# Performance work log

Hardware: AMD Instinct MI355X
Metric: run time of the kernel (lower is better)

The kernel has to match this reference:

```python
import jax, jax.numpy as jnp
import numpy as np

N_NODES = 30000
N_EDGES = 480000
N_GRAPHS = 64
NEG_SLOPE = 0.2


def gat_layer(h, src, dst, W, a_l, a_r, b):
    # h: [N, F_in], W: [F_in, H*D], a_l/a_r: [H, D], b: [H*D]
    N = h.shape[0]
    H, D = a_l.shape
    feat = (h @ W).reshape(N, H, D)
    el = jnp.sum(feat * a_l[None], axis=-1)  # [N, H]
    er = jnp.sum(feat * a_r[None], axis=-1)  # [N, H]
    e = jax.nn.leaky_relu(el[src] + er[dst], NEG_SLOPE)  # [E, H]
    # edge-softmax over incoming edges of each dst node (numerically stable)
    emax = jax.ops.segment_max(e, dst, num_segments=N)          # [N, H]
    ex = jnp.exp(e - emax[dst])                                  # [E, H]
    denom = jax.ops.segment_sum(ex, dst, num_segments=N)        # [N, H]
    alpha = ex / denom[dst]                                      # [E, H]
    msg = feat[src] * alpha[..., None]                           # [E, H, D]
    out = jax.ops.segment_sum(msg, dst, num_segments=N)         # [N, H, D]
    return out.reshape(N, H * D) + b


def setup_inputs() -> dict:
    key = jax.random.key(0)
    ks = jax.random.split(key, 16)
    feat = jax.random.normal(ks[0], (N_NODES, 6), dtype=jnp.float32)
    src = jax.random.randint(ks[1], (N_EDGES,), 0, N_NODES)
    dst = jax.random.randint(ks[2], (N_EDGES,), 0, N_NODES)
    graph_id = jnp.sort(jax.random.randint(ks[3], (N_NODES,), 0, N_GRAPHS))
    s = 0.1
    W1 = jax.random.normal(ks[4], (6, 128), dtype=jnp.float32) * s
    al1 = jax.random.normal(ks[5], (4, 32), dtype=jnp.float32) * s
    ar1 = jax.random.normal(ks[6], (4, 32), dtype=jnp.float32) * s
    b1 = jnp.zeros((128,), dtype=jnp.float32)
    W2 = jax.random.normal(ks[7], (128, 128), dtype=jnp.float32) * s
    al2 = jax.random.normal(ks[8], (4, 32), dtype=jnp.float32) * s
    ar2 = jax.random.normal(ks[9], (4, 32), dtype=jnp.float32) * s
    b2 = jnp.zeros((128,), dtype=jnp.float32)
    W3 = jax.random.normal(ks[10], (128, 256), dtype=jnp.float32) * s
    al3 = jax.random.normal(ks[11], (4, 64), dtype=jnp.float32) * s
    ar3 = jax.random.normal(ks[12], (4, 64), dtype=jnp.float32) * s
    b3 = jnp.zeros((256,), dtype=jnp.float32)
    return {"feat": feat, "src": src, "dst": dst, "graph_id": graph_id,
            "W1": W1, "al1": al1, "ar1": ar1, "b1": b1,
            "W2": W2, "al2": al2, "ar2": ar2, "b2": b2,
            "W3": W3, "al3": al3, "ar3": ar3, "b3": b3}


def reference(feat, src, dst, graph_id, W1, al1, ar1, b1, W2, al2, ar2, b2, W3, al3, ar3, b3):
    h = gat_layer(feat, src, dst, W1, al1, ar1, b1)  # [N, 128]
    h = jax.nn.relu(h)                                # dropout is identity in eval
    h = gat_layer(h, src, dst, W2, al2, ar2, b2)      # [N, 128]
    h = jax.nn.relu(h)
    h = gat_layer(h, src, dst, W3, al3, ar3, b3)      # [N, 256]
    # dgl.mean_nodes over batched graphs
    hs = jax.ops.segment_sum(h, graph_id, num_segments=N_GRAPHS)  # [G, 256]
    cnt = jax.ops.segment_sum(jnp.ones((h.shape[0],), h.dtype), graph_id, num_segments=N_GRAPHS)
    hg = hs / jnp.maximum(cnt, 1.0)[:, None]
    return hg
```

## Files before the change

### kernel.cpp

```cpp
#include <hip/hip_runtime.h>

typedef _Float16 h4 __attribute__((ext_vector_type(4)));
typedef _Float16 h8v __attribute__((ext_vector_type(8)));
typedef float f4v __attribute__((ext_vector_type(4)));
typedef float f32x8 __attribute__((ext_vector_type(8)));


__global__ void zero_i32(int* __restrict__ p, int n) {
    int i = blockIdx.x * blockDim.x + threadIdx.x;
    if (i < n) p[i] = 0;
}

__global__ void hist_kernel(const int* __restrict__ dst, int* __restrict__ counts, int E) {
    int i = blockIdx.x * blockDim.x + threadIdx.x;
    if (i < E) atomicAdd(&counts[dst[i]], 1);
}

__global__ void scan_block(const int* __restrict__ counts, int* __restrict__ rowptr,
                           int* __restrict__ bsum, int n) {
    __shared__ int wsum[16];
    const int tid = threadIdx.x;
    const int lane = tid & 63, wv = tid >> 6;
    const int i = blockIdx.x * 1024 + tid;
    int v = (i < n) ? counts[i] : 0;
    int x = v;
#pragma unroll
    for (int off = 1; off < 64; off <<= 1) {
        int t = __shfl_up(x, off);
        if (lane >= off) x += t;
    }
    if (lane == 63) wsum[wv] = x;
    __syncthreads();
    if (tid < 16) {
        int y = wsum[tid];
#pragma unroll
        for (int off = 1; off < 16; off <<= 1) {
            int t = __shfl_up(y, off);
            if (tid >= off) y += t;
        }
        wsum[tid] = y;
    }
    __syncthreads();
    int woff = (wv > 0) ? wsum[wv - 1] : 0;
    if (i < n) rowptr[i] = woff + x - v;
    if (tid == 0) bsum[blockIdx.x] = wsum[15];
}

__global__ void scan_add_tops(int* __restrict__ rowptr, const int* __restrict__ bsum,
                              int nb, int n) {
    __shared__ int off_s, tot_s;
    const int b = blockIdx.x;
    const int tid = threadIdx.x;
    if (tid < 64) {
        int v = (tid < nb) ? bsum[tid] : 0;
        int x = v;
#pragma unroll
        for (int off = 1; off < 64; off <<= 1) {
            int t = __shfl_up(x, off);
            if (tid >= off) x += t;
        }
        if (tid == 63) tot_s = x;
        if (tid == b) off_s = x - v;
    }
    __syncthreads();
    int i = b * 1024 + tid;
    if (i < n) rowptr[i] += off_s;
    if (b == 0 && tid == 0) rowptr[n] = tot_s;
}

__global__ void scatter_kernel(const int* __restrict__ src, const int* __restrict__ dst,
                               const int* __restrict__ rowptr, int* __restrict__ cursor,
                               int* __restrict__ srcs, int E) {
    int i = blockIdx.x * blockDim.x + threadIdx.x;
    if (i < E) {
        int d = dst[i];
        int p = rowptr[d] + atomicAdd(&cursor[d], 1);
        srcs[p] = src[i];
    }
}

__global__ void pack_w_both(const float* __restrict__ W2, _Float16* __restrict__ Wp2,
                            const float* __restrict__ W3, _Float16* __restrict__ Wp3) {
    int idx = blockIdx.x * blockDim.x + threadIdx.x;
    const float* W; _Float16* Wp; int FOUT;
    if (idx < 2048) { W = W2; Wp = Wp2; FOUT = 128; }
    else {
        idx -= 2048;
        if (idx >= 4096) return;
        W = W3; Wp = Wp3; FOUT = 256;
    }
    int l = idx & 63;
    int ks = (idx >> 6) & 3;
    int ct = idx >> 8;
    int kbase = ks * 32 + (l >> 4) * 8;
    int col = ct * 16 + (l & 15);
    h8v v;
#pragma unroll
    for (int e = 0; e < 8; e++) v[e] = (_Float16)W[(size_t)(kbase + e) * FOUT + col];
    *reinterpret_cast<h8v*>(&Wp[(size_t)idx * 8]) = v;
}

template <int FIN, int FOUT, int D>
__global__ void gemm_att(const float* __restrict__ A, const float* __restrict__ W,
                         const float* __restrict__ al, const float* __restrict__ ar,
                         _Float16* __restrict__ feat, float* __restrict__ el,
                         float* __restrict__ er, int N) {
    constexpr int R = 16;
    constexpr int H = FOUT / D;
    constexpr int T = FOUT / 2;
    __shared__ __align__(16) float As[FIN][R + 4];
    const int j = threadIdx.x;
    const int h0 = j / D;
    const int h1 = (j + T) / D;
    const float alv0 = al[j],     arv0 = ar[j];
    const float alv1 = al[j + T], arv1 = ar[j + T];
    const int row0 = blockIdx.x * R;

    for (int idx = threadIdx.x; idx < R * FIN; idx += T) {
        int r = idx / FIN, k = idx % FIN;
        int rr = row0 + r;
        As[k][r] = (rr < N) ? A[(size_t)rr * FIN + k] : 0.f;
    }
    __syncthreads();

    float acc0[R], acc1[R];
#pragma unroll
    for (int r = 0; r < R; r++) { acc0[r] = 0.f; acc1[r] = 0.f; }

    for (int k = 0; k < FIN; k++) {
        float w0 = W[(size_t)k * FOUT + j];
        float w1 = W[(size_t)k * FOUT + j + T];
        const float4* ap = reinterpret_cast<const float4*>(&As[k][0]);
        float av[16];
        *reinterpret_cast<float4*>(&av[0])  = ap[0];
        *reinterpret_cast<float4*>(&av[4])  = ap[1];
        *reinterpret_cast<float4*>(&av[8])  = ap[2];
        *reinterpret_cast<float4*>(&av[12]) = ap[3];
#pragma unroll
        for (int r = 0; r < R; r++) {
            acc0[r] += av[r] * w0;
            acc1[r] += av[r] * w1;
        }
    }

#pragma unroll
    for (int r = 0; r < R; r++) {
        int rr = row0 + r;
        if (rr >= N) break;
        float v0 = acc0[r], v1 = acc1[r];
        feat[(size_t)rr * FOUT + j] = (_Float16)v0;
        feat[(size_t)rr * FOUT + j + T] = (_Float16)v1;
        float vl0 = v0 * alv0, vr0 = v0 * arv0;
        float vl1 = v1 * alv1, vr1 = v1 * arv1;
#pragma unroll
        for (int off = D / 2; off >= 1; off >>= 1) {
            vl0 += __shfl_xor(vl0, off);
            vr0 += __shfl_xor(vr0, off);
            vl1 += __shfl_xor(vl1, off);
            vr1 += __shfl_xor(vr1, off);
        }
        if ((j % D) == 0) {
            el[(size_t)rr * H + h0] = vl0;
            er[(size_t)rr * H + h0] = vr0;
            el[(size_t)rr * H + h1] = vl1;
            er[(size_t)rr * H + h1] = vr1;
        }
    }
}

template <int K, int FOUT, int D>
__global__ __launch_bounds__(256)
void gemm_mfma(const _Float16* __restrict__ A, const _Float16* __restrict__ Wp,
               const float* __restrict__ al, const float* __restrict__ ar,
               _Float16* __restrict__ feat, float* __restrict__ el,
               float* __restrict__ er, int N) {
    constexpr int RB  = 32;
    constexpr int KS  = K / 32;
    constexpr int CHW = FOUT / 2;
    constexpr int CTW = CHW / 16;
    constexpr int CTH = D / 16;
    constexpr int HW  = CTW / CTH;
    constexpr int H   = FOUT / D;
    constexpr int STR = K + 8;
    __shared__ _Float16 As[RB * STR];
    const int tid = threadIdx.x;
    const int w  = tid >> 6;
    const int l  = tid & 63;
    const int rt = w >> 1;
    const int ch = w & 1;
    const int row0 = blockIdx.x * RB;

    constexpr int NV8 = RB * K / 8;
    for (int v = tid; v < NV8; v += 256) {
        int r  = v / (K / 8);
        int kv = (v % (K / 8)) * 8;
        int rr = row0 + r;
        h8v x = {};
        if (rr < N) x = *reinterpret_cast<const h8v*>(&A[(size_t)rr * K + kv]);
        *reinterpret_cast<h8v*>(&As[r * STR + kv]) = x;
    }
    __syncthreads();

    h8v afrag[KS];
    {
        const _Float16* base = &As[(rt * 16 + (l & 15)) * STR + ((l >> 4) * 8)];
#pragma unroll
        for (int ks = 0; ks < KS; ks++)
            afrag[ks] = *reinterpret_cast<const h8v*>(&base[ks * 32]);
    }

    const h8v* Wv = reinterpret_cast<const h8v*>(Wp);
    const int ct0 = ch * CTW;
    f4v acc[CTW];
#pragma unroll
    for (int c = 0; c < CTW; c++) acc[c] = (f4v){0.f, 0.f, 0.f, 0.f};

    h8v bfr[2][KS];
#pragma unroll
    for (int ks = 0; ks < KS; ks++) bfr[0][ks] = Wv[(size_t)((ct0 * KS + ks) * 64 + l)];
#pragma unroll
    for (int c = 0; c < CTW; c++) {
        const int cur = c & 1, nxt = cur ^ 1;
        if (c + 1 < CTW) {
#pragma unroll
            for (int ks = 0; ks < KS; ks++)
                bfr[nxt][ks] = Wv[(size_t)(((ct0 + c + 1) * KS + ks) * 64 + l)];
        }
#pragma unroll
        for (int ks = 0; ks < KS; ks++)
            acc[c] = __builtin_amdgcn_mfma_f32_16x16x32_f16(afrag[ks], bfr[cur][ks], acc[c], 0, 0, 0);
    }

    float elp[HW][4], erp[HW][4];
#pragma unroll
    for (int hh = 0; hh < HW; hh++)
#pragma unroll
        for (int r = 0; r < 4; r++) { elp[hh][r] = 0.f; erp[hh][r] = 0.f; }

#pragma unroll
    for (int c = 0; c < CTW; c++) {
        const int col = ch * CHW + c * 16 + (l & 15);
        const float alv = al[col], arv = ar[col];
        const int hh = c / CTH;
#pragma unroll
        for (int r = 0; r < 4; r++) {
            float v = acc[c][r];
            elp[hh][r] += v * alv;
            erp[hh][r] += v * arv;
            int rr = row0 + rt * 16 + (l >> 4) * 4 + r;
            if (rr < N) feat[(size_t)rr * FOUT + col] = (_Float16)v;
        }
    }
#pragma unroll
    for (int hh = 0; hh < HW; hh++) {
#pragma unroll
        for (int r = 0; r < 4; r++) {
            float v = elp[hh][r], u = erp[hh][r];
#pragma unroll
            for (int off = 8; off >= 1; off >>= 1) {
                v += __shfl_xor(v, off);
                u += __shfl_xor(u, off);
            }
            if ((l & 15) == 0) {
                int rr = row0 + rt * 16 + (l >> 4) * 4 + r;
                if (rr < N) {
                    int hg = ch * HW + hh;
                    el[(size_t)rr * H + hg] = v;
                    er[(size_t)rr * H + hg] = u;
                }
            }
        }
    }
}

template <int HD, int D, bool FP16OUT>
__global__ __launch_bounds__(256)
void agg_fused(const h8v* __restrict__ featH8, const float* __restrict__ el,
               const float* __restrict__ er, const int* __restrict__ srcs,
               const int* __restrict__ rowptr, const float* __restrict__ bias,
               void* __restrict__ outp, int N) {
    constexpr int TPN = HD / 8;
    constexpr int NPB = 256 / TPN;
    const int tid = threadIdx.x;
    const int ln = tid % TPN;
    const int node = blockIdx.x * NPB + tid / TPN;
    if (node >= N) return;
    const int h = ln / (D / 8);
    const int beg = rowptr[node], end = rowptr[node + 1];
    const float ern = er[(size_t)node * 4 + h];

    float s = 0.f;
    f32x8 a0 = {0,0,0,0,0,0,0,0}, a1 = a0;

    int i = beg;
    int alend = (beg + 3) & ~3;
    if (alend > end) alend = end;
    for (; i < alend; i++) {
        int u = srcs[i];
        float x = el[(size_t)u * 4 + h] + ern; x = x > 0.f ? x : 0.2f * x;
        h8v f = featH8[(size_t)u * TPN + ln];
        float w = __expf(x);
        s += w;
#pragma unroll
        for (int k = 0; k < 8; k++) a0[k] += w * (float)f[k];
    }
    for (; i + 4 <= end; i += 4) {
        int4 uu = *reinterpret_cast<const int4*>(&srcs[i]);
        float x0 = el[(size_t)uu.x * 4 + h] + ern; x0 = x0 > 0.f ? x0 : 0.2f * x0;
        float x1 = el[(size_t)uu.y * 4 + h] + ern; x1 = x1 > 0.f ? x1 : 0.2f * x1;
        float x2 = el[(size_t)uu.z * 4 + h] + ern; x2 = x2 > 0.f ? x2 : 0.2f * x2;
        float x3 = el[(size_t)uu.w * 4 + h] + ern; x3 = x3 > 0.f ? x3 : 0.2f * x3;
        h8v f0 = featH8[(size_t)uu.x * TPN + ln];
        h8v f1 = featH8[(size_t)uu.y * TPN + ln];
        h8v f2 = featH8[(size_t)uu.z * TPN + ln];
        h8v f3 = featH8[(size_t)uu.w * TPN + ln];
        float w0 = __expf(x0), w1 = __expf(x1);
        float w2 = __expf(x2), w3 = __expf(x3);
        s += (w0 + w1) + (w2 + w3);
#pragma unroll
        for (int k = 0; k < 8; k++) {
            a0[k] += w0 * (float)f0[k];
            a1[k] += w1 * (float)f1[k];
            a0[k] += w2 * (float)f2[k];
            a1[k] += w3 * (float)f3[k];
        }
    }
    for (; i < end; i++) {
        int u = srcs[i];
        float x = el[(size_t)u * 4 + h] + ern; x = x > 0.f ? x : 0.2f * x;
        h8v f = featH8[(size_t)u * TPN + ln];
        float w = __expf(x);
        s += w;
#pragma unroll
        for (int k = 0; k < 8; k++) a0[k] += w * (float)f[k];
    }
    const float inv = (s > 0.f) ? 1.f / s : 0.f;
    if constexpr (FP16OUT) {
        const float4 b0 = *reinterpret_cast<const float4*>(&bias[ln * 8]);
        const float4 b1v = *reinterpret_cast<const float4*>(&bias[ln * 8 + 4]);
        float bb[8] = {b0.x, b0.y, b0.z, b0.w, b1v.x, b1v.y, b1v.z, b1v.w};
        h8v o;
#pragma unroll
        for (int k = 0; k < 8; k++)
            o[k] = (_Float16)fmaxf((a0[k] + a1[k]) * inv + bb[k], 0.f);
        reinterpret_cast<h8v*>(outp)[(size_t)node * TPN + ln] = o;
    } else {
        f32x8 o;
#pragma unroll
        for (int k = 0; k < 8; k++) o[k] = (a0[k] + a1[k]) * inv;
        reinterpret_cast<f32x8*>(outp)[(size_t)node * TPN + ln] = o;
    }
}


__device__ __forceinline__ int lower_bound_i(const int* __restrict__ a, int n, int key) {
    int lo = 0, hi = n;
    while (lo < hi) {
        int mid = (lo + hi) >> 1;
        if (a[mid] < key) lo = mid + 1; else hi = mid;
    }
    return lo;
}

__global__ void readout_partial(const float* __restrict__ agg, const int* __restrict__ gid,
                                float* __restrict__ part, int N, int C, int SL) {
    int g = blockIdx.x / SL, slice = blockIdx.x % SL;
    int c = threadIdx.x;
    int start = lower_bound_i(gid, N, g);
    int end = lower_bound_i(gid, N, g + 1);
    float sum = 0.f;
    for (int n = start + slice; n < end; n += SL) sum += agg[(size_t)n * C + c];
    part[((size_t)g * SL + slice) * C + c] = sum;
}

__global__ void readout_final(const float* __restrict__ part, const float* __restrict__ b3,
                              const int* __restrict__ gid, float* __restrict__ out,
                              int N, int C, int SL) {
    int g = blockIdx.x, c = threadIdx.x;
    int start = lower_bound_i(gid, N, g);
    int end = lower_bound_i(gid, N, g + 1);
    int cnt = end - start;
    float s = 0.f;
    for (int k = 0; k < SL; k++) s += part[((size_t)g * SL + k) * C + c];
    out[(size_t)g * C + c] = (cnt > 0) ? s / (float)cnt + b3[c] : 0.f;
}


extern "C" void kernel_launch(void* const* d_in, const int* in_sizes, int n_in,
                              void* d_out, int out_size, void* d_ws, size_t ws_size,
                              hipStream_t stream) {
    const float* feat0 = (const float*)d_in[0];
    const int* src = (const int*)d_in[1];
    const int* dst = (const int*)d_in[2];
    const int* gid = (const int*)d_in[3];
    const float* W1 = (const float*)d_in[4];
    const float* al1 = (const float*)d_in[5];
    const float* ar1 = (const float*)d_in[6];
    const float* b1 = (const float*)d_in[7];
    const float* W2 = (const float*)d_in[8];
    const float* al2 = (const float*)d_in[9];
    const float* ar2 = (const float*)d_in[10];
    const float* b2 = (const float*)d_in[11];
    const float* W3 = (const float*)d_in[12];
    const float* al3 = (const float*)d_in[13];
    const float* ar3 = (const float*)d_in[14];
    const float* b3 = (const float*)d_in[15];

    const int N = in_sizes[0] / 6;
    const int E = in_sizes[1];
    const int G = 64;
    const int SL = 8;
    float* out = (float*)d_out;

    char* wsp = (char*)d_ws;
    auto alloc = [&](size_t bytes) -> char* {
        char* p = wsp;
        wsp += (bytes + 255) & ~(size_t)255;
        return p;
    };
    int* counts   = (int*)alloc((size_t)N * 4);
    int* rowptr   = (int*)alloc((size_t)(N + 1) * 4);
    int* cursor   = (int*)alloc((size_t)N * 4);
    int* bsum     = (int*)alloc(64 * 4);
    int* srcs     = (int*)alloc((size_t)E * 4);
    float* el     = (float*)alloc((size_t)N * 4 * 4);
    float* er     = (float*)alloc((size_t)N * 4 * 4);
    _Float16* featH = (_Float16*)alloc((size_t)N * 256 * 2);
    _Float16* aggH  = (_Float16*)alloc((size_t)N * 128 * 2);
    float* aggB   = (float*)alloc((size_t)N * 256 * 4);
    float* part   = (float*)alloc((size_t)G * SL * 256 * 4);
    _Float16* Wp2 = (_Float16*)alloc((size_t)128 * 128 * 2);
    _Float16* Wp3 = (_Float16*)alloc((size_t)128 * 256 * 2);

    const int nb = (N + 1023) / 1024;
    const int zspan = (int)(((char*)bsum - (char*)counts) / 4) + 64;
    zero_i32<<<dim3((zspan + 255) / 256), dim3(256), 0, stream>>>(counts, zspan);
    hist_kernel<<<dim3((E + 255) / 256), dim3(256), 0, stream>>>(dst, counts, E);
    scan_block<<<dim3(nb), dim3(1024), 0, stream>>>(counts, rowptr, bsum, N);
    scan_add_tops<<<dim3(nb), dim3(1024), 0, stream>>>(rowptr, bsum, nb, N);
    scatter_kernel<<<dim3((E + 255) / 256), dim3(256), 0, stream>>>(
        src, dst, rowptr, cursor, srcs, E);

    pack_w_both<<<dim3(24), dim3(256), 0, stream>>>(W2, Wp2, W3, Wp3);

    gemm_att<6, 128, 32><<<dim3((N + 15) / 16), dim3(64), 0, stream>>>(
        feat0, W1, al1, ar1, featH, el, er, N);
    agg_fused<128, 32, true><<<dim3((N + 15) / 16), dim3(256), 0, stream>>>(
        (const h8v*)featH, el, er, srcs, rowptr, b1, aggH, N);

    gemm_mfma<128, 128, 32><<<dim3((N + 31) / 32), dim3(256), 0, stream>>>(
        aggH, Wp2, al2, ar2, featH, el, er, N);
    agg_fused<128, 32, true><<<dim3((N + 15) / 16), dim3(256), 0, stream>>>(
        (const h8v*)featH, el, er, srcs, rowptr, b2, aggH, N);

    gemm_mfma<128, 256, 64><<<dim3((N + 31) / 32), dim3(256), 0, stream>>>(
        aggH, Wp3, al3, ar3, featH, el, er, N);
    agg_fused<256, 64, false><<<dim3((N + 7) / 8), dim3(256), 0, stream>>>(
        (const h8v*)featH, el, er, srcs, rowptr, nullptr, aggB, N);

    readout_partial<<<dim3(G * SL), dim3(256), 0, stream>>>(aggB, gid, part, N, 256, SL);
    readout_final<<<dim3(G), dim3(256), 0, stream>>>(part, b3, gid, out, N, 256, SL);
}
```

Baseline: 209.9 us.

## Fuse front kernels, split aggregation by channel sections, store layer-3 output in fp16

Merges the histogram, weight-packing and first-layer GEMM into a single launch using block-index ranges, which removes two launches. The edge aggregation kernels now split the channels into 2 or 4 sections across blocks, so each thread group handles fewer channels and more nodes. This is meant to improve gather locality and occupancy, at the cost of reading edge lists and attention logits once per section. The final aggregation output becomes fp16 instead of fp32, halving its write and readout traffic at some cost in precision.

```diff
diff --git a/kernel.cpp b/kernel.cpp
--- a/kernel.cpp
+++ b/kernel.cpp
@@ -9,11 +9,6 @@
 __global__ void zero_i32(int* __restrict__ p, int n) {
     int i = blockIdx.x * blockDim.x + threadIdx.x;
     if (i < n) p[i] = 0;
-}
-
-__global__ void hist_kernel(const int* __restrict__ dst, int* __restrict__ counts, int E) {
-    int i = blockIdx.x * blockDim.x + threadIdx.x;
-    if (i < E) atomicAdd(&counts[dst[i]], 1);
 }
 
 __global__ void scan_block(const int* __restrict__ counts, int* __restrict__ rowptr,
@@ -79,47 +74,54 @@
     }
 }
 
-__global__ void pack_w_both(const float* __restrict__ W2, _Float16* __restrict__ Wp2,
-                            const float* __restrict__ W3, _Float16* __restrict__ Wp3) {
-    int idx = blockIdx.x * blockDim.x + threadIdx.x;
-    const float* W; _Float16* Wp; int FOUT;
-    if (idx < 2048) { W = W2; Wp = Wp2; FOUT = 128; }
-    else {
-        idx -= 2048;
-        if (idx >= 4096) return;
-        W = W3; Wp = Wp3; FOUT = 256;
-    }
-    int l = idx & 63;
-    int ks = (idx >> 6) & 3;
-    int ct = idx >> 8;
-    int kbase = ks * 32 + (l >> 4) * 8;
-    int col = ct * 16 + (l & 15);
-    h8v v;
-#pragma unroll
-    for (int e = 0; e < 8; e++) v[e] = (_Float16)W[(size_t)(kbase + e) * FOUT + col];
-    *reinterpret_cast<h8v*>(&Wp[(size_t)idx * 8]) = v;
-}
-
-template <int FIN, int FOUT, int D>
-__global__ void gemm_att(const float* __restrict__ A, const float* __restrict__ W,
-                         const float* __restrict__ al, const float* __restrict__ ar,
-                         _Float16* __restrict__ feat, float* __restrict__ el,
-                         float* __restrict__ er, int N) {
-    constexpr int R = 16;
-    constexpr int H = FOUT / D;
-    constexpr int T = FOUT / 2;
-    __shared__ __align__(16) float As[FIN][R + 4];
-    const int j = threadIdx.x;
+__global__ __launch_bounds__(256)
+void fused_front(const int* __restrict__ dst, int* __restrict__ counts, int E,
+                 const float* __restrict__ W2, _Float16* __restrict__ Wp2,
+                 const float* __restrict__ W3, _Float16* __restrict__ Wp3,
+                 const float* __restrict__ A, const float* __restrict__ W1,
+                 const float* __restrict__ al, const float* __restrict__ ar,
+                 _Float16* __restrict__ feat, float* __restrict__ el,
+                 float* __restrict__ er, int N, int HB, int PB) {
+    const int b = blockIdx.x;
+    if (b < HB) {
+        int i = b * 256 + threadIdx.x;
+        if (i < E) atomicAdd(&counts[dst[i]], 1);
+        return;
+    }
+    if (b < HB + PB) {
+        int idx = (b - HB) * 256 + threadIdx.x;
+        const float* W; _Float16* Wp; int FOUT;
+        if (idx < 2048) { W = W2; Wp = Wp2; FOUT = 128; }
+        else {
+            idx -= 2048;
+            if (idx >= 4096) return;
+            W = W3; Wp = Wp3; FOUT = 256;
+        }
+        int l = idx & 63;
+        int ks = (idx >> 6) & 3;
+        int ct = idx >> 8;
+        int kbase = ks * 32 + (l >> 4) * 8;
+        int col = ct * 16 + (l & 15);
+        h8v v;
+#pragma unroll
+        for (int e = 0; e < 8; e++) v[e] = (_Float16)W[(size_t)(kbase + e) * FOUT + col];
+        *reinterpret_cast<h8v*>(&Wp[(size_t)idx * 8]) = v;
+        return;
+    }
+    constexpr int FIN = 6, FOUT = 128, D = 32, R = 16, H = 4, T = 64;
+    __shared__ __align__(16) float As[4][FIN][R + 4];
+    const int sub = threadIdx.x >> 6;
+    const int j = threadIdx.x & 63;
     const int h0 = j / D;
     const int h1 = (j + T) / D;
     const float alv0 = al[j],     arv0 = ar[j];
     const float alv1 = al[j + T], arv1 = ar[j + T];
-    const int row0 = blockIdx.x * R;
-
-    for (int idx = threadIdx.x; idx < R * FIN; idx += T) {
+    const int row0 = (b - HB - PB) * 64 + sub * R;
+
+    for (int idx = j; idx < R * FIN; idx += T) {
         int r = idx / FIN, k = idx % FIN;
         int rr = row0 + r;
-        As[k][r] = (rr < N) ? A[(size_t)rr * FIN + k] : 0.f;
+        As[sub][k][r] = (rr < N) ? A[(size_t)rr * FIN + k] : 0.f;
     }
     __syncthreads();
 
@@ -128,9 +130,9 @@
     for (int r = 0; r < R; r++) { acc0[r] = 0.f; acc1[r] = 0.f; }
 
     for (int k = 0; k < FIN; k++) {
-        float w0 = W[(size_t)k * FOUT + j];
-        float w1 = W[(size_t)k * FOUT + j + T];
-        const float4* ap = reinterpret_cast<const float4*>(&As[k][0]);
+        float w0 = W1[(size_t)k * FOUT + j];
+        float w1 = W1[(size_t)k * FOUT + j + T];
+        const float4* ap = reinterpret_cast<const float4*>(&As[sub][k][0]);
         float av[16];
         *reinterpret_cast<float4*>(&av[0])  = ap[0];
         *reinterpret_cast<float4*>(&av[4])  = ap[1];
@@ -273,21 +275,25 @@
     }
 }
 
-template <int HD, int D, bool FP16OUT>
+template <int HD, int D, int CSPLIT, bool FP16OUT>
 __global__ __launch_bounds__(256)
 void agg_fused(const h8v* __restrict__ featH8, const float* __restrict__ el,
                const float* __restrict__ er, const int* __restrict__ srcs,
                const int* __restrict__ rowptr, const float* __restrict__ bias,
-               void* __restrict__ outp, int N) {
-    constexpr int TPN = HD / 8;
+               void* __restrict__ outp, int N, int nbase) {
+    constexpr int CH  = HD / CSPLIT;
+    constexpr int TPN = CH / 8;
     constexpr int NPB = 256 / TPN;
     const int tid = threadIdx.x;
     const int ln = tid % TPN;
-    const int node = blockIdx.x * NPB + tid / TPN;
+    const int sec = blockIdx.x / nbase;
+    const int node = (blockIdx.x % nbase) * NPB + tid / TPN;
     if (node >= N) return;
-    const int h = ln / (D / 8);
+    const int chbase = sec * CH;
+    const int h = (chbase + ln * 8) / D;
     const int beg = rowptr[node], end = rowptr[node + 1];
     const float ern = er[(size_t)node * 4 + h];
+    const h8v* frow = featH8 + (chbase / 8) + ln;
 
     float s = 0.f;
     f32x8 a0 = {0,0,0,0,0,0,0,0}, a1 = a0;
@@ -298,7 +304,7 @@
     for (; i < alend; i++) {
         int u = srcs[i];
         float x = el[(size_t)u * 4 + h] + ern; x = x > 0.f ? x : 0.2f * x;
-        h8v f = featH8[(size_t)u * TPN + ln];
+        h8v f = frow[(size_t)u * (HD / 8)];
         float w = __expf(x);
         s += w;
 #pragma unroll
@@ -310,10 +316,10 @@
         float x1 = el[(size_t)uu.y * 4 + h] + ern; x1 = x1 > 0.f ? x1 : 0.2f * x1;
         float x2 = el[(size_t)uu.z * 4 + h] + ern; x2 = x2 > 0.f ? x2 : 0.2f * x2;
         float x3 = el[(size_t)uu.w * 4 + h] + ern; x3 = x3 > 0.f ? x3 : 0.2f * x3;
-        h8v f0 = featH8[(size_t)uu.x * TPN + ln];
-        h8v f1 = featH8[(size_t)uu.y * TPN + ln];
-        h8v f2 = featH8[(size_t)uu.z * TPN + ln];
-        h8v f3 = featH8[(size_t)uu.w * TPN + ln];
+        h8v f0 = frow[(size_t)uu.x * (HD / 8)];
+        h8v f1 = frow[(size_t)uu.y * (HD / 8)];
+        h8v f2 = frow[(size_t)uu.z * (HD / 8)];
+        h8v f3 = frow[(size_t)uu.w * (HD / 8)];
         float w0 = __expf(x0), w1 = __expf(x1);
         float w2 = __expf(x2), w3 = __expf(x3);
         s += (w0 + w1) + (w2 + w3);
@@ -328,7 +334,7 @@
     for (; i < end; i++) {
         int u = srcs[i];
         float x = el[(size_t)u * 4 + h] + ern; x = x > 0.f ? x : 0.2f * x;
-        h8v f = featH8[(size_t)u * TPN + ln];
+        h8v f = frow[(size_t)u * (HD / 8)];
         float w = __expf(x);
         s += w;
 #pragma unroll
@@ -336,19 +342,19 @@
     }
     const float inv = (s > 0.f) ? 1.f / s : 0.f;
     if constexpr (FP16OUT) {
-        const float4 b0 = *reinterpret_cast<const float4*>(&bias[ln * 8]);
-        const float4 b1v = *reinterpret_cast<const float4*>(&bias[ln * 8 + 4]);
+        const float4 b0 = *reinterpret_cast<const float4*>(&bias[chbase + ln * 8]);
+        const float4 b1v = *reinterpret_cast<const float4*>(&bias[chbase + ln * 8 + 4]);
         float bb[8] = {b0.x, b0.y, b0.z, b0.w, b1v.x, b1v.y, b1v.z, b1v.w};
         h8v o;
 #pragma unroll
         for (int k = 0; k < 8; k++)
             o[k] = (_Float16)fmaxf((a0[k] + a1[k]) * inv + bb[k], 0.f);
-        reinterpret_cast<h8v*>(outp)[(size_t)node * TPN + ln] = o;
+        reinterpret_cast<h8v*>(outp)[(size_t)node * (HD / 8) + chbase / 8 + ln] = o;
     } else {
-        f32x8 o;
-#pragma unroll
-        for (int k = 0; k < 8; k++) o[k] = (a0[k] + a1[k]) * inv;
-        reinterpret_cast<f32x8*>(outp)[(size_t)node * TPN + ln] = o;
+        h8v o;
+#pragma unroll
+        for (int k = 0; k < 8; k++) o[k] = (_Float16)((a0[k] + a1[k]) * inv);
+        reinterpret_cast<h8v*>(outp)[(size_t)node * (HD / 8) + chbase / 8 + ln] = o;
     }
 }
 
@@ -362,14 +368,14 @@
     return lo;
 }
 
-__global__ void readout_partial(const float* __restrict__ agg, const int* __restrict__ gid,
+__global__ void readout_partial(const _Float16* __restrict__ agg, const int* __restrict__ gid,
                                 float* __restrict__ part, int N, int C, int SL) {
     int g = blockIdx.x / SL, slice = blockIdx.x % SL;
     int c = threadIdx.x;
     int start = lower_bound_i(gid, N, g);
     int end = lower_bound_i(gid, N, g + 1);
     float sum = 0.f;
-    for (int n = start + slice; n < end; n += SL) sum += agg[(size_t)n * C + c];
+    for (int n = start + slice; n < end; n += SL) sum += (float)agg[(size_t)n * C + c];
     part[((size_t)g * SL + slice) * C + c] = sum;
 }
 
@@ -427,37 +433,47 @@
     float* er     = (float*)alloc((size_t)N * 4 * 4);
     _Float16* featH = (_Float16*)alloc((size_t)N * 256 * 2);
     _Float16* aggH  = (_Float16*)alloc((size_t)N * 128 * 2);
-    float* aggB   = (float*)alloc((size_t)N * 256 * 4);
+    _Float16* aggF  = (_Float16*)alloc((size_t)N * 256 * 2);
     float* part   = (float*)alloc((size_t)G * SL * 256 * 4);
     _Float16* Wp2 = (_Float16*)alloc((size_t)128 * 128 * 2);
     _Float16* Wp3 = (_Float16*)alloc((size_t)128 * 256 * 2);
 
     const int nb = (N + 1023) / 1024;
     const int zspan = (int)(((char*)bsum - (char*)counts) / 4) + 64;
+    const int HB = (E + 255) / 256;
+    const int PB = 24;
+    const int CB = (N + 63) / 64;
+
     zero_i32<<<dim3((zspan + 255) / 256), dim3(256), 0, stream>>>(counts, zspan);
-    hist_kernel<<<dim3((E + 255) / 256), dim3(256), 0, stream>>>(dst, counts, E);
+    fused_front<<<dim3(HB + PB + CB), dim3(256), 0, stream>>>(
+        dst, counts, E, W2, Wp2, W3, Wp3, feat0, W1, al1, ar1, featH, el, er, N, HB, PB);
     scan_block<<<dim3(nb), dim3(1024), 0, stream>>>(counts, rowptr, bsum, N);
     scan_add_tops<<<dim3(nb), dim3(1024), 0, stream>>>(rowptr, bsum, nb, N);
     scatter_kernel<<<dim3((E + 255) / 256), dim3(256), 0, stream>>>(
         src, dst, rowptr, cursor, srcs, E);
 
-    pack_w_both<<<dim3(24), dim3(256), 0, stream>>>(W2, Wp2, W3, Wp3);
-
-    gemm_att<6, 128, 32><<<dim3((N + 15) / 16), dim3(64), 0, stream>>>(
-        feat0, W1, al1, ar1, featH, el, er, N);
-    agg_fused<128, 32, true><<<dim3((N + 15) / 16), dim3(256), 0, stream>>>(
-        (const h8v*)featH, el, er, srcs, rowptr, b1, aggH, N);
+    {
+        const int nbase = (N + 31) / 32;
+        agg_fused<128, 32, 2, true><<<dim3(2 * nbase), dim3(256), 0, stream>>>(
+            (const h8v*)featH, el, er, srcs, rowptr, b1, aggH, N, nbase);
+    }
 
     gemm_mfma<128, 128, 32><<<dim3((N + 31) / 32), dim3(256), 0, stream>>>(
         aggH, Wp2, al2, ar2, featH, el, er, N);
-    agg_fused<128, 32, true><<<dim3((N + 15) / 16), dim3(256), 0, stream>>>(
-        (const h8v*)featH, el, er, srcs, rowptr, b2, aggH, N);
+    {
+        const int nbase = (N + 31) / 32;
+        agg_fused<128, 32, 2, true><<<dim3(2 * nbase), dim3(256), 0, stream>>>(
+            (const h8v*)featH, el, er, srcs, rowptr, b2, aggH, N, nbase);
+    }
 
     gemm_mfma<128, 256, 64><<<dim3((N + 31) / 32), dim3(256), 0, stream>>>(
         aggH, Wp3, al3, ar3, featH, el, er, N);
-    agg_fused<256, 64, false><<<dim3((N + 7) / 8), dim3(256), 0, stream>>>(
-        (const h8v*)featH, el, er, srcs, rowptr, nullptr, aggB, N);
-
-    readout_partial<<<dim3(G * SL), dim3(256), 0, stream>>>(aggB, gid, part, N, 256, SL);
+    {
+        const int nbase = (N + 31) / 32;
+        agg_fused<256, 64, 4, false><<<dim3(4 * nbase), dim3(256), 0, stream>>>(
+            (const h8v*)featH, el, er, srcs, rowptr, nullptr, aggF, N, nbase);
+    }
+
+    readout_partial<<<dim3(G * SL), dim3(256), 0, stream>>>(aggF, gid, part, N, 256, SL);
     readout_final<<<dim3(G), dim3(256), 0, stream>>>(part, b3, gid, out, N, 256, SL);
 }
```

After: 214.8 us. 1.02x slower.
